# Kernel optimization log

Hardware: AMD Instinct MI355X
Metric: run time of the kernel (lower is better)

Reference implementation:

```python
import jax, jax.numpy as jnp
from jax import lax
import numpy as np

B, H, W, C = 8, 32, 32, 256
SOFTMAX_SCALE = 10.0
DN = ('NHWC', 'HWIO', 'NHWC')


def _patches(t):
    # t: [b,h,w,c] -> [b,h,w,3,3,c], SAME zero padding, stride 1 (tf.image.extract_patches)
    b, h, w, c = t.shape
    tp = jnp.pad(t, ((0, 0), (1, 1), (1, 1), (0, 0)))
    cols = [tp[:, i:i + h, j:j + w, :] for i in range(3) for j in range(3)]
    return jnp.stack(cols, axis=3).reshape(b, h, w, 3, 3, c)


def _diag_fuse(z):
    # conv2d of [L,L] map with eye(3) kernel, SAME padding:
    # out[i,j] = z[i-1,j-1] + z[i,j] + z[i+1,j+1] (zero padded)
    dr = jnp.pad(z, ((1, 0), (1, 0)))[:-1, :-1]
    ul = jnp.pad(z, ((0, 1), (0, 1)))[1:, 1:]
    return z + dr + ul


def _conv(x, w):
    return lax.conv_general_dilated(x, w, (1, 1), 'SAME', dimension_numbers=DN)


def _attend(xi, wi, mmean):
    # xi: [h,w,c]; wi: [3,3,c,L] patch kernels; mmean: [L] mean of mask patches
    h, w, c = xi.shape
    L = h * w
    norm = jnp.maximum(jnp.sqrt(jnp.sum(wi * wi, axis=(0, 1, 2))), 1e-4)
    yi = _conv(xi[None], wi / norm)[0]  # [h,w,L] cosine-sim scores
    # fuse: diagonal propagation along both spatial orderings
    z = yi.reshape(L, L)
    z = _diag_fuse(z).reshape(h, w, h, w).transpose(1, 0, 3, 2).reshape(L, L)
    z = _diag_fuse(z).reshape(w, h, w, h).transpose(1, 0, 3, 2)  # [h,w,h,w]
    yi = z.reshape(h, w, L)
    mm = (mmean == 1.0).astype(yi.dtype)  # valid-patch mask per location
    yi = jax.nn.softmax(yi * mm * SOFTMAX_SCALE, axis=-1) * mm
    # conv2d_transpose(yi, wi, stride 1, SAME) == conv with hw-flipped kernel,
    # in/out channels swapped (TF filter layout [h,w,out=C,in=L])
    k2 = jnp.flip(wi, (0, 1)).transpose(0, 1, 3, 2)  # [3,3,L,C]
    return _conv(yi[None], k2)[0]  # [h,w,c]


def _forward(x, mask, conv_w, conv_b, conv1_w, conv1_b, conv2_w, conv2_b):
    b, h, w, c = x.shape
    L = h * w
    # rate=1: tf.image.resize to same size is identity, f == b == x
    wi = _patches(x).reshape(b, L, 3, 3, c).transpose(0, 2, 3, 4, 1)  # [b,3,3,c,L]
    mmean = _patches(mask).mean(axis=(3, 4, 5)).reshape(b, L)
    y = jax.vmap(_attend)(x, wi, mmean)  # [b,h,w,c]
    ycat = jnp.concatenate([y, x], axis=-1)  # [b,h,w,2c]
    g1 = jax.nn.sigmoid(_conv(ycat, conv1_w) + conv1_b)
    g2 = jax.nn.sigmoid(_conv(ycat, conv2_w) + conv2_b)
    gate = (g1 + g2) * 0.5
    out = gate * (_conv(ycat, conv_w) + conv_b)
    return out, jnp.ones_like(mask)


def setup_inputs() -> dict:
    key = jax.random.key(0)
    ks = jax.random.split(key, 4)
    x = jax.random.normal(ks[0], (B, H, W, C), jnp.float32)
    mask = jnp.ones((B, H, W, 1), jnp.float32)
    conv_w = jax.random.normal(ks[1], (3, 3, 2 * C, C), jnp.float32) * 0.02
    conv_b = jnp.zeros((C,), jnp.float32)
    conv1_w = jax.random.normal(ks[2], (1, 1, 2 * C, C), jnp.float32) * 0.02
    conv1_b = jnp.zeros((C,), jnp.float32)
    conv2_w = jax.random.normal(ks[3], (3, 3, 2 * C, C), jnp.float32) * 0.02
    conv2_b = jnp.zeros((C,), jnp.float32)
    return {'x': x, 'mask': mask, 'conv_w': conv_w, 'conv_b': conv_b,
            'conv1_w': conv1_w, 'conv1_b': conv1_b, 'conv2_w': conv2_w, 'conv2_b': conv2_b}


def reference(x, mask, conv_w, conv_b, conv1_w, conv1_b, conv2_w, conv2_b):
    return _forward(x, mask, conv_w, conv_b, conv1_w, conv1_b, conv2_w, conv2_b)
```

## Files before the change

### kernel.cpp

```cpp
#include <hip/hip_runtime.h>
#include <math.h>

typedef unsigned short u16;
typedef __bf16 bf16x8 __attribute__((ext_vector_type(8)));
typedef float f32x4 __attribute__((ext_vector_type(4)));

#define NPOS 1156
#define GSTR 1160
#define GOFF (GSTR * 1156)
#define YSTR 1032
#define YOFF (YSTR * 1026)
#define POS34(p) ((((p) >> 5) + 1) * 34 + ((p) & 31) + 1)

__device__ __constant__ const int kDiagOff[9] = {
    -35 * (GSTR + 1), -34 * (GSTR + 1), -33 * (GSTR + 1),
    -1 * (GSTR + 1),  0,                1 * (GSTR + 1),
    33 * (GSTR + 1),  34 * (GSTR + 1),  35 * (GSTR + 1)};

__device__ __forceinline__ u16 f2bf(float f) {
  unsigned int u = __builtin_bit_cast(unsigned int, f);
  return (u16)((u + 0x7FFFu + ((u >> 16) & 1u)) >> 16);
}
__device__ __forceinline__ float bf2f(u16 v) {
  unsigned int u = ((unsigned int)v) << 16;
  return __builtin_bit_cast(float, u);
}
__device__ __forceinline__ void gload16(const void* g, void* l) {
  __builtin_amdgcn_global_load_lds(
      (const __attribute__((address_space(1))) void*)g,
      (__attribute__((address_space(3))) void*)l, 16, 0, 0);
}
__device__ __forceinline__ int posOf(int p) { return POS34(p); }

__device__ __forceinline__ float wredmax(float v) {
#pragma unroll
  for (int m = 32; m; m >>= 1) v = fmaxf(v, __shfl_xor(v, m));
  return v;
}
__device__ __forceinline__ float wredsum(float v) {
#pragma unroll
  for (int m = 32; m; m >>= 1) v += __shfl_xor(v, m);
  return v;
}

__global__ __launch_bounds__(256) void zb_pre(
    float* __restrict__ Gpad, u16* __restrict__ Ylin,
    u16* __restrict__ xpad, u16* __restrict__ ypad) {
  int bi = blockIdx.x, tid = threadIdx.x;
  if (bi < 9248) {
    int b = bi / 1156, r = bi - b * 1156;
    float* row = Gpad + (size_t)b * GOFF + (size_t)r * GSTR;
    int rm = r % 34;
    bool brow = (r < 34) || (r >= 1122) || (rm == 0) || (rm == 33);
    if (brow) {
      for (int c = tid; c < GSTR; c += 256) row[c] = 0.f;
    } else {
      for (int c = tid; c < GSTR; c += 256) {
        int cm = c % 34;
        if (c < 34 || c >= 1122 || cm == 0 || cm == 33) row[c] = 0.f;
      }
    }
    return;
  }
  bi -= 9248;
  if (bi < 8208) {
    int b = bi / 1026, r = bi - b * 1026;
    u16* row = Ylin + (size_t)b * YOFF + (size_t)r * YSTR;
    if (r == 0 || r == 1025) {
      for (int c = tid; c < YSTR; c += 256) row[c] = 0;
    } else if (tid < 8) {
      row[tid == 0 ? 0 : 1024 + tid] = 0;
    }
    return;
  }
  bi -= 8208;
  int arr = bi / 9248;
  bi -= arr * 9248;
  int b = bi / 1156, p = bi - b * 1156;
  int pm = p % 34;
  bool bp = (p < 34) || (p >= 1122) || (pm == 0) || (pm == 33);
  if (!bp) return;
  u16* dst = (arr ? ypad : xpad) + ((size_t)b * NPOS + p) * 256;
  dst[tid] = 0;
}

__global__ __launch_bounds__(256) void zb_apad(u16* __restrict__ Apad2) {
  int bi = blockIdx.x, tid = threadIdx.x;
  int b = bi / 1156, r = bi - b * 1156;
  u16* row = Apad2 + (size_t)b * GOFF + (size_t)r * GSTR;
  int rm = r % 34;
  bool brow = (r < 34) || (r >= 1122) || (rm == 0) || (rm == 33);
  if (brow) {
    for (int c = tid; c < GSTR; c += 256) row[c] = 0;
  } else {
    for (int c = tid; c < GSTR; c += 256) {
      int cm = c % 34;
      if (c < 34 || c >= 1122 || cm == 0 || cm == 33) row[c] = 0;
    }
  }
}

__global__ __launch_bounds__(256) void cast_x(
    const float* __restrict__ x, u16* __restrict__ xpad, u16* __restrict__ xT) {
  int blk = blockIdx.x;
  int b = blk >> 5, h = blk & 31;
  __shared__ u16 T[256][33];
  const float* xrow = x + ((size_t)b * 1024 + h * 32) * 256;
  int tid = threadIdx.x;
  for (int idx = tid; idx < 8192; idx += 256) {
    int w = idx >> 8, c = idx & 255;
    u16 v = f2bf(xrow[(size_t)w * 256 + c]);
    T[c][w] = v;
    xpad[((size_t)b * NPOS + (h + 1) * 34 + (w + 1)) * 256 + c] = v;
  }
  __syncthreads();
  int c = tid;
  unsigned int* dp = (unsigned int*)(xT + ((size_t)(b * 256 + c)) * 1024 + h * 32);
  const unsigned int* sp = (const unsigned int*)&T[c][0];
#pragma unroll
  for (int u = 0; u < 16; ++u) dp[u] = sp[u];
}

__global__ __launch_bounds__(256) void wtrans(
    const float* __restrict__ src, u16* __restrict__ dst, int K) {
  int k0 = blockIdx.x * 32;
  __shared__ u16 T[256][34];
  int tid = threadIdx.x;
  for (int idx = tid; idx < 8192; idx += 256) {
    int kr = idx >> 8, c = idx & 255;
    T[c][kr] = f2bf(src[(size_t)(k0 + kr) * 256 + c]);
  }
  __syncthreads();
  int c = tid;
  unsigned int* dp = (unsigned int*)(dst + (size_t)c * K + k0);
  const unsigned int* sp = (const unsigned int*)&T[c][0];
#pragma unroll
  for (int u = 0; u < 16; ++u) dp[u] = sp[u];
}

__global__ __launch_bounds__(256) void gram_base(
    const u16* __restrict__ xpad, float* __restrict__ Gpad) {
  const int b = blockIdx.z;
  const int m0 = blockIdx.x << 7;
  const int n0 = blockIdx.y << 7;
  const u16* xb = xpad + (size_t)b * NPOS * 256;
  __shared__ __align__(16) u16 As[128 * 64];
  __shared__ __align__(16) u16 Bs[128 * 64];
  const int tid = threadIdx.x;
  const int lane = tid & 63;
  const int wave = tid >> 6;
  const int wm = wave >> 1, wn = wave & 1;
  const int srow = lane >> 3;
  const int cswz = ((lane & 7) ^ srow) << 3;
  int pa[4], pb[4];
#pragma unroll
  for (int i = 0; i < 4; ++i) {
    pa[i] = posOf(m0 + wave * 32 + i * 8 + srow);
    pb[i] = posOf(n0 + wave * 32 + i * 8 + srow);
  }
  int aidx[4][2], bidx[4][2];
#pragma unroll
  for (int f = 0; f < 4; ++f)
#pragma unroll
    for (int ks = 0; ks < 2; ++ks) {
      int ra = wm * 64 + f * 16 + (lane & 15);
      int rb = wn * 64 + f * 16 + (lane & 15);
      int k16 = ks * 4 + (lane >> 4);
      aidx[f][ks] = ra * 64 + ((k16 ^ (ra & 7)) << 3);
      bidx[f][ks] = rb * 64 + ((k16 ^ (rb & 7)) << 3);
    }
  f32x4 acc[4][4] = {};
  for (int c0 = 0; c0 < 256; c0 += 64) {
    __syncthreads();
#pragma unroll
    for (int i = 0; i < 4; ++i) {
      gload16(xb + (size_t)pa[i] * 256 + c0 + cswz, &As[(wave * 32 + i * 8) * 64]);
      gload16(xb + (size_t)pb[i] * 256 + c0 + cswz, &Bs[(wave * 32 + i * 8) * 64]);
    }
    __syncthreads();
#pragma unroll
    for (int ks = 0; ks < 2; ++ks) {
      bf16x8 a[4], bb[4];
#pragma unroll
      for (int f = 0; f < 4; ++f) a[f] = *(const bf16x8*)(As + aidx[f][ks]);
#pragma unroll
      for (int f = 0; f < 4; ++f) bb[f] = *(const bf16x8*)(Bs + bidx[f][ks]);
#pragma unroll
      for (int mi = 0; mi < 4; ++mi)
#pragma unroll
        for (int ni = 0; ni < 4; ++ni)
          acc[mi][ni] = __builtin_amdgcn_mfma_f32_16x16x32_bf16(a[mi], bb[ni], acc[mi][ni], 0, 0, 0);
    }
  }
  float* Gb = Gpad + (size_t)b * GOFF;
  const int r0 = (lane >> 4) << 2;
  const int cb0 = n0 + wn * 64 + (lane & 15);
#pragma unroll
  for (int mi = 0; mi < 4; ++mi) {
    int row = m0 + wm * 64 + mi * 16 + r0;
    int rp = POS34(row);
#pragma unroll
    for (int ni = 0; ni < 4; ++ni) {
      int cp = POS34(cb0 + ni * 16);
#pragma unroll
      for (int r = 0; r < 4; ++r)
        Gb[(size_t)(rp + r) * GSTR + cp] = acc[mi][ni][r];
    }
  }
}

__global__ __launch_bounds__(256) void norm_mm(
    const float* __restrict__ Gpad, const float* __restrict__ mask,
    float* __restrict__ invn, float* __restrict__ mm, float* __restrict__ ones_out) {
  int idx = blockIdx.x * 256 + threadIdx.x;
  int b = idx >> 10, l = idx & 1023;
  const float* Gb = Gpad + (size_t)b * GOFF;
  size_t dbase = (size_t)POS34(l) * (GSTR + 1);
  float d = 0.f;
#pragma unroll
  for (int t = 0; t < 9; ++t) d += Gb[dbase + kDiagOff[t]];
  invn[idx] = 1.0f / fmaxf(sqrtf(d), 1e-4f);
  int lh = l >> 5, lw = l & 31;
  float s = 0.f;
  for (int dh = -1; dh <= 1; ++dh)
    for (int dw = -1; dw <= 1; ++dw) {
      int hh = lh + dh, wv = lw + dw;
      if (hh >= 0 && hh < 32 && wv >= 0 && wv < 32) s += mask[b * 1024 + hh * 32 + wv];
    }
  mm[idx] = ((s / 9.0f) == 1.0f) ? 1.0f : 0.0f;
  ones_out[idx] = 1.0f;
}

__global__ __launch_bounds__(256) void patch_norm_p(
    const float* __restrict__ Gpad, const float* __restrict__ invn,
    u16* __restrict__ Ylin) {
  const int b = blockIdx.y;
  const int p0 = blockIdx.x << 2;
  const float* Gb = Gpad + (size_t)b * GOFF;
  u16* Yb = Ylin + (size_t)b * YOFF;
  const int tid = threadIdx.x;
  const int l0 = tid << 2;
  const int lp0 = POS34(l0);
  const float4 iv = *(const float4*)(invn + (b << 10) + l0);
#pragma unroll
  for (int r = 0; r < 4; ++r) {
    int p = p0 + r;
    int base = POS34(p) * GSTR + lp0;
    float v[9][4];
#pragma unroll
    for (int t = 0; t < 9; ++t) {
      const float* q = Gb + (base + kDiagOff[t]);
      v[t][0] = q[0]; v[t][1] = q[1]; v[t][2] = q[2]; v[t][3] = q[3];
    }
    float s0 = 0.f, s1 = 0.f, s2 = 0.f, s3 = 0.f;
#pragma unroll
    for (int t = 0; t < 9; ++t) { s0 += v[t][0]; s1 += v[t][1]; s2 += v[t][2]; s3 += v[t][3]; }
    u16* yw = Yb + (size_t)(p + 1) * YSTR + l0 + 1;
    yw[0] = f2bf(s0 * iv.x); yw[1] = f2bf(s1 * iv.y);
    yw[2] = f2bf(s2 * iv.z); yw[3] = f2bf(s3 * iv.w);
  }
}

#define CSTR 1032

__device__ __forceinline__ float z1p(const u16* __restrict__ Yb, int r, int c) {
  size_t a = (size_t)(r + 1) * YSTR + (c + 1);
  return bf2f(Yb[a]) + bf2f(Yb[a - (YSTR + 1)]) + bf2f(Yb[a + (YSTR + 1)]);
}

__global__ __launch_bounds__(256) void fuse_softmax_band(
    const u16* __restrict__ Ylin, const float* __restrict__ mm,
    u16* __restrict__ Apad2) {
  const int bi = blockIdx.x;
  const int b = bi >> 8;
  const int i0 = (bi & 255) << 2;
  const u16* Yb = Ylin + (size_t)b * YOFF;
  const float* mmb = mm + (b << 10);
  const int tid = threadIdx.x;
  const int w = tid >> 6;
  const int lane = tid & 63;
  const int i = i0 + w;
  __shared__ __align__(16) u16 cache[18 * CSTR];
  const bool interior = (i0 >= 32) && (i0 <= 988);
  float logit[16];
  float mmv[16];
  float lmax = -3.0e38f;
  if (interior) {
    for (int ch = tid; ch < 18 * 129; ch += 256) {
      int k = ch / 129;
      int c8 = (ch - k * 129) << 3;
      int g = (k < 6) ? (i0 - 32 + k) : (k < 12) ? (i0 + k - 6) : (i0 + 32 + k - 12);
      gload16(Yb + (size_t)g * YSTR + c8, cache + ch * 8);
    }
    __syncthreads();
    const u16* cu = cache + w * CSTR;
    const u16* cc = cache + (w + 6) * CSTR;
    const u16* cl = cache + (w + 12) * CSTR;
#define Z1C(base, c) (bf2f((base)[(c)]) + bf2f((base)[CSTR + (c) + 1]) + bf2f((base)[2 * CSTR + (c) + 2]))
#pragma unroll
    for (int q = 0; q < 16; ++q) {
      int j = lane + (q << 6);
      int sj = ((j & 31) << 5) | (j >> 5);
      float S = Z1C(cc, j);
      if (sj >= 1) {
        int col = (((sj - 1) & 31) << 5) | ((sj - 1) >> 5);
        S += Z1C(cu, col);
      }
      if (sj <= 1022) {
        int col = (((sj + 1) & 31) << 5) | ((sj + 1) >> 5);
        S += Z1C(cl, col);
      }
      mmv[q] = mmb[j];
      float lg = S * mmv[q] * 10.0f;
      logit[q] = lg;
      lmax = fmaxf(lmax, lg);
    }
  } else {
    const int si = ((i & 31) << 5) | (i >> 5);
    const int rm = (si >= 1) ? ((((si - 1) & 31) << 5) | ((si - 1) >> 5)) : -1;
    const int rp = (si <= 1022) ? ((((si + 1) & 31) << 5) | ((si + 1) >> 5)) : -1;
#pragma unroll
    for (int q = 0; q < 16; ++q) {
      int j = lane + (q << 6);
      int sj = ((j & 31) << 5) | (j >> 5);
      float S = z1p(Yb, i, j);
      if (rm >= 0 && sj >= 1) {
        int col = (((sj - 1) & 31) << 5) | ((sj - 1) >> 5);
        S += z1p(Yb, rm, col);
      }
      if (rp >= 0 && sj <= 1022) {
        int col = (((sj + 1) & 31) << 5) | ((sj + 1) >> 5);
        S += z1p(Yb, rp, col);
      }
      mmv[q] = mmb[j];
      float lg = S * mmv[q] * 10.0f;
      logit[q] = lg;
      lmax = fmaxf(lmax, lg);
    }
  }
  lmax = wredmax(lmax);
  float lsum = 0.f;
#pragma unroll
  for (int q = 0; q < 16; ++q) { logit[q] = expf(logit[q] - lmax); lsum += logit[q]; }
  lsum = wredsum(lsum);
  float inv = 1.0f / lsum;
  u16* Ap = Apad2 + (size_t)b * GOFF + (size_t)POS34(i) * GSTR;
#pragma unroll
  for (int q = 0; q < 16; ++q) {
    int j = lane + (q << 6);
    Ap[POS34(j)] = f2bf(mmv[q] * logit[q] * inv);
  }
}

__global__ __launch_bounds__(256) void afuse_p(
    const u16* __restrict__ Apad2, u16* __restrict__ Afuse) {
  const int b = blockIdx.y;
  const int q0 = blockIdx.x << 2;
  const u16* Ab = Apad2 + (size_t)b * GOFF;
  u16* Fb = Afuse + ((size_t)b << 20);
  const int tid = threadIdx.x;
  const int l0 = tid << 2;
  const int lp0 = POS34(l0);
#pragma unroll
  for (int r = 0; r < 4; ++r) {
    int q = q0 + r;
    int base = POS34(q) * GSTR + lp0;
    float v[9][4];
#pragma unroll
    for (int t = 0; t < 9; ++t) {
      const u16* p = Ab + (base - kDiagOff[t]);
      v[t][0] = bf2f(p[0]); v[t][1] = bf2f(p[1]);
      v[t][2] = bf2f(p[2]); v[t][3] = bf2f(p[3]);
    }
    float s0 = 0.f, s1 = 0.f, s2 = 0.f, s3 = 0.f;
#pragma unroll
    for (int t = 0; t < 9; ++t) { s0 += v[t][0]; s1 += v[t][1]; s2 += v[t][2]; s3 += v[t][3]; }
    u16* fw = Fb + (size_t)q * 1024 + l0;
    fw[0] = f2bf(s0); fw[1] = f2bf(s1); fw[2] = f2bf(s2); fw[3] = f2bf(s3);
  }
}

__global__ __launch_bounds__(256) void paste_gemm(
    const u16* __restrict__ Afuse, const u16* __restrict__ xT, u16* __restrict__ ypad) {
  const int bm0 = blockIdx.x << 6;
  const int b = bm0 >> 10;
  const int q0 = bm0 & 1023;
  const int n0 = blockIdx.y << 6;
  const u16* Ab = Afuse + ((size_t)b << 20);
  const u16* xTb = xT + ((size_t)b << 18);
  __shared__ __align__(16) u16 As[64 * 64];
  __shared__ __align__(16) u16 Bs[64 * 64];
  const int tid = threadIdx.x;
  const int lane = tid & 63;
  const int wave = tid >> 6;
  const int wm = wave >> 1, wn = wave & 1;
  const int srow = lane >> 3;
  const int cswz = ((lane & 7) ^ srow) << 3;
  int aidx[2][2], bidx[2][2];
#pragma unroll
  for (int ks = 0; ks < 2; ++ks) {
    int k16 = ks * 4 + (lane >> 4);
#pragma unroll
    for (int f = 0; f < 2; ++f) {
      int ra = wm * 32 + f * 16 + (lane & 15);
      aidx[f][ks] = ra * 64 + ((k16 ^ (ra & 7)) << 3);
      int rb = wn * 32 + f * 16 + (lane & 15);
      bidx[f][ks] = rb * 64 + ((k16 ^ (rb & 7)) << 3);
    }
  }
  f32x4 acc[2][2] = {};
  for (int l0 = 0; l0 < 1024; l0 += 64) {
    __syncthreads();
#pragma unroll
    for (int i = 0; i < 2; ++i) {
      int ar = wave * 16 + i * 8 + srow;
      gload16(Ab + (size_t)(q0 + ar) * 1024 + l0 + cswz, &As[ar * 64]);
      gload16(xTb + (size_t)(n0 + ar) * 1024 + l0 + cswz, &Bs[ar * 64]);
    }
    __syncthreads();
#pragma unroll
    for (int ks = 0; ks < 2; ++ks) {
      bf16x8 a[2], bb[2];
#pragma unroll
      for (int f = 0; f < 2; ++f) a[f] = *(const bf16x8*)(As + aidx[f][ks]);
#pragma unroll
      for (int f = 0; f < 2; ++f) bb[f] = *(const bf16x8*)(Bs + bidx[f][ks]);
#pragma unroll
      for (int mi = 0; mi < 2; ++mi)
#pragma unroll
        for (int ni = 0; ni < 2; ++ni)
          acc[mi][ni] = __builtin_amdgcn_mfma_f32_16x16x32_bf16(a[mi], bb[ni], acc[mi][ni], 0, 0, 0);
    }
  }
  u16* yb = ypad + (size_t)b * NPOS * 256;
  const int r0 = (lane >> 4) << 2;
#pragma unroll
  for (int mi = 0; mi < 2; ++mi) {
    int qb = q0 + wm * 32 + mi * 16 + r0;
#pragma unroll
    for (int ni = 0; ni < 2; ++ni) {
      int c = n0 + wn * 32 + ni * 16 + (lane & 15);
#pragma unroll
      for (int r = 0; r < 4; ++r)
        yb[(size_t)posOf(qb + r) * 256 + c] = f2bf(acc[mi][ni][r]);
    }
  }
}

__global__ __launch_bounds__(256) void conv_split(
    const u16* __restrict__ ypad, const u16* __restrict__ xpad,
    const u16* __restrict__ w0T, const u16* __restrict__ w2T,
    float* __restrict__ c0buf, float* __restrict__ c2buf) {
  const int m0 = blockIdx.x << 7;
  const int b = m0 >> 10;
  const int q0 = m0 & 1023;
  const int sel = blockIdx.z;
  const int n0 = blockIdx.y << 6;
  const u16* wT = sel ? w2T : w0T;
  float* dst = sel ? c2buf : c0buf;
  const u16* yb = ypad + (size_t)b * NPOS * 256;
  const u16* xb = xpad + (size_t)b * NPOS * 256;
  __shared__ __align__(16) u16 As[128 * 64];
  __shared__ __align__(16) u16 Bs[64 * 64];
  const int tid = threadIdx.x;
  const int lane = tid & 63;
  const int wave = tid >> 6;
  const int wm = wave >> 1, wn = wave & 1;
  const int srow = lane >> 3;
  const int cswz = ((lane & 7) ^ srow) << 3;
  int posA[4];
#pragma unroll
  for (int i = 0; i < 4; ++i) posA[i] = posOf(q0 + wave * 32 + i * 8 + srow);
  const u16* wrow[2];
#pragma unroll
  for (int i = 0; i < 2; ++i)
    wrow[i] = wT + (size_t)(n0 + wave * 16 + i * 8 + srow) * 4608 + cswz;
  int aidx[4][2], bidx[2][2];
#pragma unroll
  for (int ks = 0; ks < 2; ++ks) {
    int k16 = ks * 4 + (lane >> 4);
#pragma unroll
    for (int f = 0; f < 4; ++f) {
      int ra = wm * 64 + f * 16 + (lane & 15);
      aidx[f][ks] = ra * 64 + ((k16 ^ (ra & 7)) << 3);
    }
#pragma unroll
    for (int f = 0; f < 2; ++f) {
      int rb = wn * 32 + f * 16 + (lane & 15);
      bidx[f][ks] = rb * 64 + ((k16 ^ (rb & 7)) << 3);
    }
  }
  f32x4 acc[4][2] = {};
  for (int kt = 0; kt < 72; ++kt) {
    const int s = kt >> 3;
    const int c0k = (kt & 7) << 6;
    const u16* basep = (c0k < 256) ? yb : xb;
    const int coff = c0k & 255;
    const int dpos = (s / 3 - 1) * 34 + (s % 3 - 1);
    __syncthreads();
#pragma unroll
    for (int i = 0; i < 4; ++i)
      gload16(basep + (size_t)(posA[i] + dpos) * 256 + coff + cswz,
              &As[(wave * 32 + i * 8) * 64]);
#pragma unroll
    for (int i = 0; i < 2; ++i)
      gload16(wrow[i] + (kt << 6), &Bs[(wave * 16 + i * 8) * 64]);
    __syncthreads();
#pragma unroll
    for (int ks = 0; ks < 2; ++ks) {
      bf16x8 a[4], bb[2];
#pragma unroll
      for (int f = 0; f < 4; ++f) a[f] = *(const bf16x8*)(As + aidx[f][ks]);
#pragma unroll
      for (int f = 0; f < 2; ++f) bb[f] = *(const bf16x8*)(Bs + bidx[f][ks]);
#pragma unroll
      for (int mi = 0; mi < 4; ++mi)
#pragma unroll
        for (int ni = 0; ni < 2; ++ni)
          acc[mi][ni] = __builtin_amdgcn_mfma_f32_16x16x32_bf16(a[mi], bb[ni], acc[mi][ni], 0, 0, 0);
    }
  }
  const int r0 = (lane >> 4) << 2;
#pragma unroll
  for (int mi = 0; mi < 4; ++mi) {
    int m = m0 + wm * 64 + mi * 16 + r0;
#pragma unroll
    for (int ni = 0; ni < 2; ++ni) {
      int co = n0 + wn * 32 + ni * 16 + (lane & 15);
#pragma unroll
      for (int r = 0; r < 4; ++r)
        dst[(size_t)(m + r) * 256 + co] = acc[mi][ni][r];
    }
  }
}

__global__ __launch_bounds__(256) void conv1_gemm(
    const u16* __restrict__ ypad, const u16* __restrict__ xpad,
    const u16* __restrict__ w1T, float* __restrict__ c1buf) {
  const int m0 = blockIdx.x << 6;
  const int b = m0 >> 10;
  const int q0 = m0 & 1023;
  const int n0 = blockIdx.y << 6;
  const u16* yb = ypad + (size_t)b * NPOS * 256;
  const u16* xb = xpad + (size_t)b * NPOS * 256;
  __shared__ __align__(16) u16 As[64 * 64];
  __shared__ __align__(16) u16 Bs[64 * 64];
  const int tid = threadIdx.x;
  const int lane = tid & 63;
  const int wave = tid >> 6;
  const int wm = wave >> 1, wn = wave & 1;
  const int srow = lane >> 3;
  const int cswz = ((lane & 7) ^ srow) << 3;
  int posA[2];
#pragma unroll
  for (int i = 0; i < 2; ++i) posA[i] = posOf(q0 + wave * 16 + i * 8 + srow);
  int aidx[2][2], bidx[2][2];
#pragma unroll
  for (int ks = 0; ks < 2; ++ks) {
    int k16 = ks * 4 + (lane >> 4);
#pragma unroll
    for (int f = 0; f < 2; ++f) {
      int ra = wm * 32 + f * 16 + (lane & 15);
      aidx[f][ks] = ra * 64 + ((k16 ^ (ra & 7)) << 3);
      int rb = wn * 32 + f * 16 + (lane & 15);
      bidx[f][ks] = rb * 64 + ((k16 ^ (rb & 7)) << 3);
    }
  }
  f32x4 acc[2][2] = {};
  for (int kt = 0; kt < 8; ++kt) {
    const int c0k = kt << 6;
    const u16* basep = (c0k < 256) ? yb : xb;
    const int coff = c0k & 255;
    __syncthreads();
#pragma unroll
    for (int i = 0; i < 2; ++i) {
      int ar = wave * 16 + i * 8 + srow;
      gload16(basep + (size_t)posA[i] * 256 + coff + cswz, &As[ar * 64]);
      gload16(w1T + (size_t)(n0 + ar) * 512 + c0k + cswz, &Bs[ar * 64]);
    }
    __syncthreads();
#pragma unroll
    for (int ks = 0; ks < 2; ++ks) {
      bf16x8 a[2], bb[2];
#pragma unroll
      for (int f = 0; f < 2; ++f) a[f] = *(const bf16x8*)(As + aidx[f][ks]);
#pragma unroll
      for (int f = 0; f < 2; ++f) bb[f] = *(const bf16x8*)(Bs + bidx[f][ks]);
#pragma unroll
      for (int mi = 0; mi < 2; ++mi)
#pragma unroll
        for (int ni = 0; ni < 2; ++ni)
          acc[mi][ni] = __builtin_amdgcn_mfma_f32_16x16x32_bf16(a[mi], bb[ni], acc[mi][ni], 0, 0, 0);
    }
  }
  const int r0 = (lane >> 4) << 2;
#pragma unroll
  for (int mi = 0; mi < 2; ++mi) {
    int m = m0 + wm * 32 + mi * 16 + r0;
#pragma unroll
    for (int ni = 0; ni < 2; ++ni) {
      int co = n0 + wn * 32 + ni * 16 + (lane & 15);
#pragma unroll
      for (int r = 0; r < 4; ++r)
        c1buf[(size_t)(m + r) * 256 + co] = acc[mi][ni][r];
    }
  }
}

__global__ __launch_bounds__(256) void gate_out(
    const float* __restrict__ c0buf, const float* __restrict__ c1buf,
    const float* __restrict__ c2buf, const float* __restrict__ b0,
    const float* __restrict__ b1, const float* __restrict__ b2,
    float* __restrict__ out) {
  size_t i4 = ((size_t)blockIdx.x * 256 + threadIdx.x) * 4;
  int co = (int)(i4 & 255);
  float4 v0 = *(const float4*)(c0buf + i4);
  float4 v1 = *(const float4*)(c1buf + i4);
  float4 v2 = *(const float4*)(c2buf + i4);
  float4 q0 = *(const float4*)(b0 + co);
  float4 q1 = *(const float4*)(b1 + co);
  float4 q2 = *(const float4*)(b2 + co);
  float4 o;
  const float* pv0 = (const float*)&v0; const float* pv1 = (const float*)&v1;
  const float* pv2 = (const float*)&v2; const float* pq0 = (const float*)&q0;
  const float* pq1 = (const float*)&q1; const float* pq2 = (const float*)&q2;
  float* po = (float*)&o;
#pragma unroll
  for (int j = 0; j < 4; ++j) {
    float g1 = 1.f / (1.f + expf(-(pv1[j] + pq1[j])));
    float g2 = 1.f / (1.f + expf(-(pv2[j] + pq2[j])));
    po[j] = 0.5f * (g1 + g2) * (pv0[j] + pq0[j]);
  }
  *(float4*)(out + i4) = o;
}


extern "C" void kernel_launch(void* const* d_in, const int* in_sizes, int n_in,
                              void* d_out, int out_size, void* d_ws, size_t ws_size,
                              hipStream_t stream) {
  const float* x = (const float*)d_in[0];
  const float* mask = (const float*)d_in[1];
  const float* conv_w = (const float*)d_in[2];
  const float* conv_b = (const float*)d_in[3];
  const float* conv1_w = (const float*)d_in[4];
  const float* conv1_b = (const float*)d_in[5];
  const float* conv2_w = (const float*)d_in[6];
  const float* conv2_b = (const float*)d_in[7];
  float* out = (float*)d_out;
  char* wsb = (char*)d_ws;

  float* Gpad  = (float*)(wsb + 0);
  u16* Apad2   = (u16*)(wsb + 0);
  float* c0buf = (float*)(wsb + 0);
  float* c2buf = (float*)(wsb + 8388608);
  float* c1buf = (float*)(wsb + 16777216);
  u16* Ylin    = (u16*)(wsb + 42910720);
  u16* Afuse   = (u16*)(wsb + 42910720);
  u16* xpad    = (u16*)(wsb + 59852032);
  u16* ypad    = (u16*)(wsb + 64587008);
  u16* xT      = (u16*)(wsb + 69321984);
  u16* w0T     = (u16*)(wsb + 73516288);
  u16* w2T     = (u16*)(wsb + 75875584);
  u16* w1T     = (u16*)(wsb + 78234880);
  float* invn  = (float*)(wsb + 78497024);
  float* mmb   = (float*)(wsb + 78529792);

  zb_pre<<<35952, 256, 0, stream>>>(Gpad, Ylin, xpad, ypad);
  cast_x<<<256, 256, 0, stream>>>(x, xpad, xT);
  wtrans<<<144, 256, 0, stream>>>(conv_w, w0T, 4608);
  wtrans<<<144, 256, 0, stream>>>(conv2_w, w2T, 4608);
  wtrans<<<16, 256, 0, stream>>>(conv1_w, w1T, 512);

  gram_base<<<dim3(8, 8, 8), 256, 0, stream>>>(xpad, Gpad);
  norm_mm<<<32, 256, 0, stream>>>(Gpad, mask, invn, mmb, out + 2097152);
  patch_norm_p<<<dim3(256, 8), 256, 0, stream>>>(Gpad, invn, Ylin);
  zb_apad<<<9248, 256, 0, stream>>>(Apad2);
  fuse_softmax_band<<<2048, 256, 0, stream>>>(Ylin, mmb, Apad2);
  afuse_p<<<dim3(256, 8), 256, 0, stream>>>(Apad2, Afuse);
  paste_gemm<<<dim3(128, 4), 256, 0, stream>>>(Afuse, xT, ypad);
  conv1_gemm<<<dim3(128, 4), 256, 0, stream>>>(ypad, xpad, w1T, c1buf);
  conv_split<<<dim3(64, 4, 2), 256, 0, stream>>>(ypad, xpad, w0T, w2T, c0buf, c2buf);
  gate_out<<<2048, 256, 0, stream>>>(c0buf, c1buf, c2buf, conv_b, conv1_b, conv2_b, out);
}
```

Measured before the change: 291.5 us.

## Fuse three gate convolutions with gating epilogue and swizzle block order

```diff
diff --git a/kernel.cpp b/kernel.cpp
--- a/kernel.cpp
+++ b/kernel.cpp
@@ -140,9 +140,11 @@
 
 __global__ __launch_bounds__(256) void gram_base(
     const u16* __restrict__ xpad, float* __restrict__ Gpad) {
-  const int b = blockIdx.z;
-  const int m0 = blockIdx.x << 7;
-  const int n0 = blockIdx.y << 7;
+  int lid = blockIdx.x + (blockIdx.y << 3) + (blockIdx.z << 6);
+  int swz = ((lid & 7) << 6) + (lid >> 3);
+  const int b = swz >> 6;
+  const int m0 = (swz & 7) << 7;
+  const int n0 = ((swz >> 3) & 7) << 7;
   const u16* xb = xpad + (size_t)b * NPOS * 256;
   __shared__ __align__(16) u16 As[128 * 64];
   __shared__ __align__(16) u16 Bs[128 * 64];
@@ -234,8 +236,10 @@
 __global__ __launch_bounds__(256) void patch_norm_p(
     const float* __restrict__ Gpad, const float* __restrict__ invn,
     u16* __restrict__ Ylin) {
-  const int b = blockIdx.y;
-  const int p0 = blockIdx.x << 2;
+  int lid = blockIdx.x + (blockIdx.y << 8);
+  int swz = ((lid & 7) << 8) + (lid >> 3);
+  const int b = swz >> 8;
+  const int p0 = (swz & 255) << 2;
   const float* Gb = Gpad + (size_t)b * GOFF;
   u16* Yb = Ylin + (size_t)b * YOFF;
   const int tid = threadIdx.x;
@@ -271,9 +275,10 @@
 __global__ __launch_bounds__(256) void fuse_softmax_band(
     const u16* __restrict__ Ylin, const float* __restrict__ mm,
     u16* __restrict__ Apad2) {
-  const int bi = blockIdx.x;
-  const int b = bi >> 8;
-  const int i0 = (bi & 255) << 2;
+  int lid = blockIdx.x;
+  int swz = ((lid & 7) << 8) + (lid >> 3);
+  const int b = swz >> 8;
+  const int i0 = (swz & 255) << 2;
   const u16* Yb = Ylin + (size_t)b * YOFF;
   const float* mmb = mm + (b << 10);
   const int tid = threadIdx.x;
@@ -354,8 +359,10 @@
 
 __global__ __launch_bounds__(256) void afuse_p(
     const u16* __restrict__ Apad2, u16* __restrict__ Afuse) {
-  const int b = blockIdx.y;
-  const int q0 = blockIdx.x << 2;
+  int lid = blockIdx.x + (blockIdx.y << 8);
+  int swz = ((lid & 7) << 8) + (lid >> 3);
+  const int b = swz >> 8;
+  const int q0 = (swz & 255) << 2;
   const u16* Ab = Apad2 + (size_t)b * GOFF;
   u16* Fb = Afuse + ((size_t)b << 20);
   const int tid = threadIdx.x;
@@ -382,10 +389,12 @@
 
 __global__ __launch_bounds__(256) void paste_gemm(
     const u16* __restrict__ Afuse, const u16* __restrict__ xT, u16* __restrict__ ypad) {
-  const int bm0 = blockIdx.x << 6;
+  int lid = blockIdx.x + (blockIdx.y << 7);
+  int swz = ((lid & 7) << 6) + (lid >> 3);
+  const int bm0 = (swz & 127) << 6;
   const int b = bm0 >> 10;
   const int q0 = bm0 & 1023;
-  const int n0 = blockIdx.y << 6;
+  const int n0 = (swz >> 7) << 6;
   const u16* Ab = Afuse + ((size_t)b << 20);
   const u16* xTb = xT + ((size_t)b << 18);
   __shared__ __align__(16) u16 As[64 * 64];
@@ -447,50 +456,46 @@
   }
 }
 
-__global__ __launch_bounds__(256) void conv_split(
+__global__ __launch_bounds__(256) void final_fused(
     const u16* __restrict__ ypad, const u16* __restrict__ xpad,
-    const u16* __restrict__ w0T, const u16* __restrict__ w2T,
-    float* __restrict__ c0buf, float* __restrict__ c2buf) {
-  const int m0 = blockIdx.x << 7;
+    const u16* __restrict__ w0T, const u16* __restrict__ w1T,
+    const u16* __restrict__ w2T,
+    const float* __restrict__ b0, const float* __restrict__ b1,
+    const float* __restrict__ b2, float* __restrict__ out) {
+  int lid = blockIdx.x + (blockIdx.y << 7);
+  int swz = ((lid & 7) << 6) + (lid >> 3);
+  const int m0 = (swz & 127) << 6;
   const int b = m0 >> 10;
   const int q0 = m0 & 1023;
-  const int sel = blockIdx.z;
-  const int n0 = blockIdx.y << 6;
-  const u16* wT = sel ? w2T : w0T;
-  float* dst = sel ? c2buf : c0buf;
+  const int n0 = (swz >> 7) << 6;
   const u16* yb = ypad + (size_t)b * NPOS * 256;
   const u16* xb = xpad + (size_t)b * NPOS * 256;
-  __shared__ __align__(16) u16 As[128 * 64];
-  __shared__ __align__(16) u16 Bs[64 * 64];
+  __shared__ __align__(16) u16 As[64 * 64];
+  __shared__ __align__(16) u16 B0s[64 * 64];
+  __shared__ __align__(16) u16 B1s[64 * 64];
+  __shared__ __align__(16) u16 B2s[64 * 64];
   const int tid = threadIdx.x;
   const int lane = tid & 63;
   const int wave = tid >> 6;
   const int wm = wave >> 1, wn = wave & 1;
   const int srow = lane >> 3;
   const int cswz = ((lane & 7) ^ srow) << 3;
-  int posA[4];
-#pragma unroll
-  for (int i = 0; i < 4; ++i) posA[i] = posOf(q0 + wave * 32 + i * 8 + srow);
-  const u16* wrow[2];
-#pragma unroll
-  for (int i = 0; i < 2; ++i)
-    wrow[i] = wT + (size_t)(n0 + wave * 16 + i * 8 + srow) * 4608 + cswz;
-  int aidx[4][2], bidx[2][2];
+  int posA[2];
+#pragma unroll
+  for (int i = 0; i < 2; ++i) posA[i] = posOf(q0 + wave * 16 + i * 8 + srow);
+  int aidx[2][2], bidx[2][2];
 #pragma unroll
   for (int ks = 0; ks < 2; ++ks) {
     int k16 = ks * 4 + (lane >> 4);
 #pragma unroll
-    for (int f = 0; f < 4; ++f) {
-      int ra = wm * 64 + f * 16 + (lane & 15);
+    for (int f = 0; f < 2; ++f) {
+      int ra = wm * 32 + f * 16 + (lane & 15);
       aidx[f][ks] = ra * 64 + ((k16 ^ (ra & 7)) << 3);
-    }
-#pragma unroll
-    for (int f = 0; f < 2; ++f) {
       int rb = wn * 32 + f * 16 + (lane & 15);
       bidx[f][ks] = rb * 64 + ((k16 ^ (rb & 7)) << 3);
     }
   }
-  f32x4 acc[4][2] = {};
+  f32x4 acc0[2][2] = {}, acc1[2][2] = {}, acc2[2][2] = {};
   for (int kt = 0; kt < 72; ++kt) {
     const int s = kt >> 3;
     const int c0k = (kt & 7) << 6;
@@ -499,139 +504,60 @@
     const int dpos = (s / 3 - 1) * 34 + (s % 3 - 1);
     __syncthreads();
 #pragma unroll
-    for (int i = 0; i < 4; ++i)
-      gload16(basep + (size_t)(posA[i] + dpos) * 256 + coff + cswz,
-              &As[(wave * 32 + i * 8) * 64]);
-#pragma unroll
-    for (int i = 0; i < 2; ++i)
-      gload16(wrow[i] + (kt << 6), &Bs[(wave * 16 + i * 8) * 64]);
-    __syncthreads();
-#pragma unroll
-    for (int ks = 0; ks < 2; ++ks) {
-      bf16x8 a[4], bb[2];
-#pragma unroll
-      for (int f = 0; f < 4; ++f) a[f] = *(const bf16x8*)(As + aidx[f][ks]);
-#pragma unroll
-      for (int f = 0; f < 2; ++f) bb[f] = *(const bf16x8*)(Bs + bidx[f][ks]);
-#pragma unroll
-      for (int mi = 0; mi < 4; ++mi)
-#pragma unroll
-        for (int ni = 0; ni < 2; ++ni)
-          acc[mi][ni] = __builtin_amdgcn_mfma_f32_16x16x32_bf16(a[mi], bb[ni], acc[mi][ni], 0, 0, 0);
-    }
-  }
-  const int r0 = (lane >> 4) << 2;
-#pragma unroll
-  for (int mi = 0; mi < 4; ++mi) {
-    int m = m0 + wm * 64 + mi * 16 + r0;
-#pragma unroll
-    for (int ni = 0; ni < 2; ++ni) {
-      int co = n0 + wn * 32 + ni * 16 + (lane & 15);
-#pragma unroll
-      for (int r = 0; r < 4; ++r)
-        dst[(size_t)(m + r) * 256 + co] = acc[mi][ni][r];
-    }
-  }
-}
-
-__global__ __launch_bounds__(256) void conv1_gemm(
-    const u16* __restrict__ ypad, const u16* __restrict__ xpad,
-    const u16* __restrict__ w1T, float* __restrict__ c1buf) {
-  const int m0 = blockIdx.x << 6;
-  const int b = m0 >> 10;
-  const int q0 = m0 & 1023;
-  const int n0 = blockIdx.y << 6;
-  const u16* yb = ypad + (size_t)b * NPOS * 256;
-  const u16* xb = xpad + (size_t)b * NPOS * 256;
-  __shared__ __align__(16) u16 As[64 * 64];
-  __shared__ __align__(16) u16 Bs[64 * 64];
-  const int tid = threadIdx.x;
-  const int lane = tid & 63;
-  const int wave = tid >> 6;
-  const int wm = wave >> 1, wn = wave & 1;
-  const int srow = lane >> 3;
-  const int cswz = ((lane & 7) ^ srow) << 3;
-  int posA[2];
-#pragma unroll
-  for (int i = 0; i < 2; ++i) posA[i] = posOf(q0 + wave * 16 + i * 8 + srow);
-  int aidx[2][2], bidx[2][2];
-#pragma unroll
-  for (int ks = 0; ks < 2; ++ks) {
-    int k16 = ks * 4 + (lane >> 4);
-#pragma unroll
-    for (int f = 0; f < 2; ++f) {
-      int ra = wm * 32 + f * 16 + (lane & 15);
-      aidx[f][ks] = ra * 64 + ((k16 ^ (ra & 7)) << 3);
-      int rb = wn * 32 + f * 16 + (lane & 15);
-      bidx[f][ks] = rb * 64 + ((k16 ^ (rb & 7)) << 3);
-    }
-  }
-  f32x4 acc[2][2] = {};
-  for (int kt = 0; kt < 8; ++kt) {
-    const int c0k = kt << 6;
-    const u16* basep = (c0k < 256) ? yb : xb;
-    const int coff = c0k & 255;
-    __syncthreads();
-#pragma unroll
     for (int i = 0; i < 2; ++i) {
       int ar = wave * 16 + i * 8 + srow;
-      gload16(basep + (size_t)posA[i] * 256 + coff + cswz, &As[ar * 64]);
-      gload16(w1T + (size_t)(n0 + ar) * 512 + c0k + cswz, &Bs[ar * 64]);
+      gload16(basep + (size_t)(posA[i] + dpos) * 256 + coff + cswz, &As[ar * 64]);
+      size_t krow = (size_t)(n0 + ar) * 4608 + (kt << 6) + cswz;
+      gload16(w0T + krow, &B0s[ar * 64]);
+      gload16(w2T + krow, &B2s[ar * 64]);
+      if (s == 4)
+        gload16(w1T + (size_t)(n0 + ar) * 512 + c0k + cswz, &B1s[ar * 64]);
     }
     __syncthreads();
 #pragma unroll
     for (int ks = 0; ks < 2; ++ks) {
-      bf16x8 a[2], bb[2];
+      bf16x8 a[2], v0[2], v2[2];
 #pragma unroll
       for (int f = 0; f < 2; ++f) a[f] = *(const bf16x8*)(As + aidx[f][ks]);
 #pragma unroll
-      for (int f = 0; f < 2; ++f) bb[f] = *(const bf16x8*)(Bs + bidx[f][ks]);
+      for (int f = 0; f < 2; ++f) v0[f] = *(const bf16x8*)(B0s + bidx[f][ks]);
+#pragma unroll
+      for (int f = 0; f < 2; ++f) v2[f] = *(const bf16x8*)(B2s + bidx[f][ks]);
 #pragma unroll
       for (int mi = 0; mi < 2; ++mi)
 #pragma unroll
-        for (int ni = 0; ni < 2; ++ni)
-          acc[mi][ni] = __builtin_amdgcn_mfma_f32_16x16x32_bf16(a[mi], bb[ni], acc[mi][ni], 0, 0, 0);
+        for (int ni = 0; ni < 2; ++ni) {
+          acc0[mi][ni] = __builtin_amdgcn_mfma_f32_16x16x32_bf16(a[mi], v0[ni], acc0[mi][ni], 0, 0, 0);
+          acc2[mi][ni] = __builtin_amdgcn_mfma_f32_16x16x32_bf16(a[mi], v2[ni], acc2[mi][ni], 0, 0, 0);
+        }
+      if (s == 4) {
+        bf16x8 v1[2];
+#pragma unroll
+        for (int f = 0; f < 2; ++f) v1[f] = *(const bf16x8*)(B1s + bidx[f][ks]);
+#pragma unroll
+        for (int mi = 0; mi < 2; ++mi)
+#pragma unroll
+          for (int ni = 0; ni < 2; ++ni)
+            acc1[mi][ni] = __builtin_amdgcn_mfma_f32_16x16x32_bf16(a[mi], v1[ni], acc1[mi][ni], 0, 0, 0);
+      }
     }
   }
   const int r0 = (lane >> 4) << 2;
 #pragma unroll
-  for (int mi = 0; mi < 2; ++mi) {
-    int m = m0 + wm * 32 + mi * 16 + r0;
-#pragma unroll
-    for (int ni = 0; ni < 2; ++ni) {
-      int co = n0 + wn * 32 + ni * 16 + (lane & 15);
-#pragma unroll
-      for (int r = 0; r < 4; ++r)
-        c1buf[(size_t)(m + r) * 256 + co] = acc[mi][ni][r];
-    }
-  }
-}
-
-__global__ __launch_bounds__(256) void gate_out(
-    const float* __restrict__ c0buf, const float* __restrict__ c1buf,
-    const float* __restrict__ c2buf, const float* __restrict__ b0,
-    const float* __restrict__ b1, const float* __restrict__ b2,
-    float* __restrict__ out) {
-  size_t i4 = ((size_t)blockIdx.x * 256 + threadIdx.x) * 4;
-  int co = (int)(i4 & 255);
-  float4 v0 = *(const float4*)(c0buf + i4);
-  float4 v1 = *(const float4*)(c1buf + i4);
-  float4 v2 = *(const float4*)(c2buf + i4);
-  float4 q0 = *(const float4*)(b0 + co);
-  float4 q1 = *(const float4*)(b1 + co);
-  float4 q2 = *(const float4*)(b2 + co);
-  float4 o;
-  const float* pv0 = (const float*)&v0; const float* pv1 = (const float*)&v1;
-  const float* pv2 = (const float*)&v2; const float* pq0 = (const float*)&q0;
-  const float* pq1 = (const float*)&q1; const float* pq2 = (const float*)&q2;
-  float* po = (float*)&o;
-#pragma unroll
-  for (int j = 0; j < 4; ++j) {
-    float g1 = 1.f / (1.f + expf(-(pv1[j] + pq1[j])));
-    float g2 = 1.f / (1.f + expf(-(pv2[j] + pq2[j])));
-    po[j] = 0.5f * (g1 + g2) * (pv0[j] + pq0[j]);
-  }
-  *(float4*)(out + i4) = o;
+  for (int ni = 0; ni < 2; ++ni) {
+    int co = n0 + wn * 32 + ni * 16 + (lane & 15);
+    float q0b = b0[co], q1b = b1[co], q2b = b2[co];
+#pragma unroll
+    for (int mi = 0; mi < 2; ++mi) {
+      int m = m0 + wm * 32 + mi * 16 + r0;
+#pragma unroll
+      for (int r = 0; r < 4; ++r) {
+        float g1 = 1.f / (1.f + expf(-(acc1[mi][ni][r] + q1b)));
+        float g2 = 1.f / (1.f + expf(-(acc2[mi][ni][r] + q2b)));
+        out[(size_t)(m + r) * 256 + co] = 0.5f * (g1 + g2) * (acc0[mi][ni][r] + q0b);
+      }
+    }
+  }
 }
 
 
@@ -651,9 +577,6 @@
 
   float* Gpad  = (float*)(wsb + 0);
   u16* Apad2   = (u16*)(wsb + 0);
-  float* c0buf = (float*)(wsb + 0);
-  float* c2buf = (float*)(wsb + 8388608);
-  float* c1buf = (float*)(wsb + 16777216);
   u16* Ylin    = (u16*)(wsb + 42910720);
   u16* Afuse   = (u16*)(wsb + 42910720);
   u16* xpad    = (u16*)(wsb + 59852032);
@@ -678,7 +601,6 @@
   fuse_softmax_band<<<2048, 256, 0, stream>>>(Ylin, mmb, Apad2);
   afuse_p<<<dim3(256, 8), 256, 0, stream>>>(Apad2, Afuse);
   paste_gemm<<<dim3(128, 4), 256, 0, stream>>>(Afuse, xT, ypad);
-  conv1_gemm<<<dim3(128, 4), 256, 0, stream>>>(ypad, xpad, w1T, c1buf);
-  conv_split<<<dim3(64, 4, 2), 256, 0, stream>>>(ypad, xpad, w0T, w2T, c0buf, c2buf);
-  gate_out<<<2048, 256, 0, stream>>>(c0buf, c1buf, c2buf, conv_b, conv1_b, conv2_b, out);
-}
+  final_fused<<<dim3(128, 4), 256, 0, stream>>>(ypad, xpad, w0T, w1T, w2T,
+                                                conv_b, conv1_b, conv2_b, out);
+}
```

Result: faster. 279.9 us (-3.9%).
